# Kernel tuning notes

Measured on AMD Instinct MI355X. Metric: run time of the kernel, lower is better.

The kernel has to match this reference:

```python
import jax, jax.numpy as jnp
import numpy as np

MSE_W, SSIM_W = 0.6, 0.4
WIN, SIGMA = 11, 1.5


def _gaussian_window():
    coords = jnp.arange(WIN, dtype=jnp.float32) - (WIN - 1) / 2.0
    g = jnp.exp(-coords ** 2 / (2.0 * SIGMA ** 2))
    g = g / g.sum()
    w = jnp.outer(g, g)  # [11,11]
    return w.reshape(1, 1, WIN, WIN)  # OIHW


def _blur(x, window):
    # x: [B,1,H,W], valid conv with 11x11 gaussian
    return jax.lax.conv_general_dilated(
        x, window, window_strides=(1, 1), padding='VALID',
        dimension_numbers=('NCHW', 'OIHW', 'NCHW'))


def setup_inputs() -> dict:
    key = jax.random.key(0)
    k1, k2 = jax.random.split(key)
    pred = jax.random.uniform(k1, (32, 1, 512, 512), dtype=jnp.float32)
    target = jax.random.uniform(k2, (32, 1, 512, 512), dtype=jnp.float32)
    return {"pred": pred, "target": target}


def reference(pred, target):
    window = _gaussian_window()
    C1 = (0.01 * 1.0) ** 2
    C2 = (0.03 * 1.0) ** 2

    mse_loss = jnp.mean((pred - target) ** 2)

    mu1 = _blur(pred, window)
    mu2 = _blur(target, window)
    mu1_sq = mu1 * mu1
    mu2_sq = mu2 * mu2
    mu1_mu2 = mu1 * mu2
    sigma1_sq = _blur(pred * pred, window) - mu1_sq
    sigma2_sq = _blur(target * target, window) - mu2_sq
    sigma12 = _blur(pred * target, window) - mu1_mu2

    ssim_map = (2.0 * mu1_mu2 + C1) * (2.0 * sigma12 + C2) / (
        (mu1_sq + mu2_sq + C1) * (sigma1_sq + sigma2_sq + C2) + 1e-6)
    ssim_loss = 1.0 - jnp.mean(ssim_map)

    return MSE_W * mse_loss + SSIM_W * ssim_loss
```

## Files before the change

### kernel.cpp

```cpp
#include <hip/hip_runtime.h>
#include <math.h>

#define BATCH 32
#define H 512
#define W 512
#define OUT_HW 502
#define TS_X 32
#define BAND 32
#define NBANDS 16
#define NTX 16
#define NBLOCKS (NTX * BATCH)
#define N1 ((double)BATCH * H * W)
#define N2 ((double)BATCH * OUT_HW * OUT_HW)

#define RSTR 56
#define TSTR 56

struct GaussW { float g[11]; };

typedef _Float16 h8  __attribute__((ext_vector_type(8)));
typedef __fp16   h2t __attribute__((ext_vector_type(2)));
typedef float    f4t __attribute__((ext_vector_type(4)));

__global__ __launch_bounds__(256, 2)
void ssim_mfma_kernel(const float* __restrict__ pred,
                      const float* __restrict__ targ,
                      float* __restrict__ ws_contrib,
                      GaussW gw)
{
    __shared__ __align__(16) _Float16 raw[4][48 * RSTR];
    __shared__ __align__(16) _Float16 rbt[4][32 * TSTR];
    __shared__ float red[8];

    const int tid = threadIdx.x;
    const int bid = blockIdx.x;
    const int tx  = bid >> 5;
    const int b   = ((bid & 7) << 2) | ((bid >> 3) & 3);
    const int ox0 = tx * TS_X;
    const int cols = min(TS_X, OUT_HW - ox0);
    const bool interior_x = (ox0 + 48 <= W);

    const float* __restrict__ pb = pred + ((size_t)b << 18);
    const float* __restrict__ tb = targ + ((size_t)b << 18);

    const int lane = tid & 63, wave = tid >> 6;
    const int quad = lane >> 4, nn = lane & 15, quad8 = quad << 3;

    const int pr = tid / 6, pg = tid - pr * 6;
    const bool pactive = interior_x | (pg < 4);

    {
        _Float16* base = &raw[0][0];
        const int total = 4 * 48 * RSTR;
        for (int i = tid * 8; i < total; i += 256 * 8)
            *(f4t*)(base + i) = f4t{0.f, 0.f, 0.f, 0.f};
    }

    h8 gfrag;
    #pragma unroll
    for (int j = 0; j < 8; ++j) {
        const int kk = quad8 + j - nn;
        float val = 0.f;
        #pragma unroll
        for (int t2 = 0; t2 < 11; ++t2) val = (kk == t2) ? gw.g[t2] : val;
        gfrag[j] = (_Float16)val;
    }
    const f4t zero4 = {0.f, 0.f, 0.f, 0.f};
    const float C1 = 1e-4f, C2 = 9e-4f;

    float mse_local = 0.f, ssim_local = 0.f;

    f4t pf0, pf1, pf2, pf3;
    {
        const int nnew = 42;
        if ((tid < nnew * 6) & pactive) {
            const int base = (pr << 9) + ox0 + 8 * pg;
            pf0 = *(const f4t*)(pb + base);
            pf1 = *(const f4t*)(pb + base + 4);
            pf2 = *(const f4t*)(tb + base);
            pf3 = *(const f4t*)(tb + base + 4);
        }
    }

    __syncthreads();

    int hbase = 0, obase = 0;

    #pragma unroll 1
    for (int band = 0; band < NBANDS; ++band) {
        const int out0 = band * BAND;
        const int h0   = (band == 0) ? 0 : (out0 + 10);
        const int nnew = min(out0 + 42, H) - h0;

        if ((tid < nnew * 6) & pactive) {
            const h2t hp0 = __builtin_amdgcn_cvt_pkrtz(pf0[0], pf0[1]);
            const h2t hp1 = __builtin_amdgcn_cvt_pkrtz(pf0[2], pf0[3]);
            const h2t hp2 = __builtin_amdgcn_cvt_pkrtz(pf1[0], pf1[1]);
            const h2t hp3 = __builtin_amdgcn_cvt_pkrtz(pf1[2], pf1[3]);
            const h2t ht0 = __builtin_amdgcn_cvt_pkrtz(pf2[0], pf2[1]);
            const h2t ht1 = __builtin_amdgcn_cvt_pkrtz(pf2[2], pf2[3]);
            const h2t ht2 = __builtin_amdgcn_cvt_pkrtz(pf3[0], pf3[1]);
            const h2t ht3 = __builtin_amdgcn_cvt_pkrtz(pf3[2], pf3[3]);
            __align__(16) h2t sv[4], dv[4], ssv[4], ddv[4];
            sv[0] = hp0 + ht0; sv[1] = hp1 + ht1; sv[2] = hp2 + ht2; sv[3] = hp3 + ht3;
            dv[0] = hp0 - ht0; dv[1] = hp1 - ht1; dv[2] = hp2 - ht2; dv[3] = hp3 - ht3;
            ssv[0] = sv[0] * sv[0]; ssv[1] = sv[1] * sv[1];
            ssv[2] = sv[2] * sv[2]; ssv[3] = sv[3] * sv[3];
            ddv[0] = dv[0] * dv[0]; ddv[1] = dv[1] * dv[1];
            ddv[2] = dv[2] * dv[2]; ddv[3] = dv[3] * dv[3];

            if (pg < 4) {
                const h2t macc = (ddv[0] + ddv[1]) + (ddv[2] + ddv[3]);
                mse_local += (float)macc[0] + (float)macc[1];
            }

            int s = hbase + pr;
            s -= (s >= 48) ? 48 : 0;
            const int off = s * RSTR + 8 * pg;
            *(f4t*)&raw[0][off] = *(const f4t*)sv;
            *(f4t*)&raw[1][off] = *(const f4t*)dv;
            *(f4t*)&raw[2][off] = *(const f4t*)ssv;
            *(f4t*)&raw[3][off] = *(const f4t*)ddv;
        }
        __syncthreads();

        if (band + 1 < NBANDS) {
            const int nh0   = out0 + BAND + 10;
            const int nnnew = min(out0 + BAND + 42, H) - nh0;
            if ((tid < nnnew * 6) & pactive) {
                const int base = ((nh0 + pr) << 9) + ox0 + 8 * pg;
                pf0 = *(const f4t*)(pb + base);
                pf1 = *(const f4t*)(pb + base + 4);
                pf2 = *(const f4t*)(tb + base);
                pf3 = *(const f4t*)(tb + base + 4);
            }
        }

        #pragma unroll 1
        for (int t5 = wave; t5 < 24; t5 += 4) {
            const int ch = t5 & 3, rem = t5 >> 2;
            const int j0 = (rem & 1) << 4, r0 = (rem >> 1) << 4;
            int u = obase + r0 + nn;
            u -= (u >= 48) ? 48 : 0;
            const h8 a = *(const h8*)&raw[ch][u * RSTR + j0 + quad8];
            const f4t dacc = __builtin_amdgcn_mfma_f32_16x16x32_f16(a, gfrag, zero4, 0, 0, 0);
            h2t* wp = (h2t*)&rbt[ch][(j0 + nn) * TSTR + r0 + (quad << 2)];
            wp[0] = __builtin_amdgcn_cvt_pkrtz(dacc[0], dacc[1]);
            wp[1] = __builtin_amdgcn_cvt_pkrtz(dacc[2], dacc[3]);
        }
        __syncthreads();

        {
            const int c0 = (wave & 1) << 4, r0v = (wave >> 1) << 4;
            f4t dv2[4];
            #pragma unroll
            for (int ch = 0; ch < 4; ++ch) {
                const h8 a = *(const h8*)&rbt[ch][(c0 + nn) * TSTR + r0v + quad8];
                dv2[ch] = __builtin_amdgcn_mfma_f32_16x16x32_f16(a, gfrag, zero4, 0, 0, 0);
            }
            const int rowg = out0 + r0v + nn;
            if (rowg < OUT_HW) {
                #pragma unroll
                for (int reg = 0; reg < 4; ++reg) {
                    const int cl = c0 + (quad << 2) + reg;
                    if (cl < cols) {
                        const float A = dv2[0][reg], Bv = dv2[1][reg];
                        const float U = dv2[2][reg], V  = dv2[3][reg];
                        const float A2 = A * A, B2 = Bv * Bv;
                        const float mu12_2 = 0.5f * (A2 - B2);
                        const float musq   = 0.5f * (A2 + B2);
                        const float sig12_2 = 0.5f * (U - V) - mu12_2;
                        const float sigsum  = 0.5f * (U + V) - musq;
                        const float num = (mu12_2 + C1) * (sig12_2 + C2);
                        const float den = (musq + C1) * (sigsum + C2) + 1e-6f;
                        ssim_local += num * __builtin_amdgcn_rcpf(den);
                    }
                }
            }
        }

        hbase += nnew;  hbase -= (hbase >= 48) ? 48 : 0;
        obase += BAND;  obase -= (obase >= 48) ? 48 : 0;
    }

    #pragma unroll
    for (int off = 32; off > 0; off >>= 1) {
        ssim_local += __shfl_down(ssim_local, off, 64);
        mse_local  += __shfl_down(mse_local,  off, 64);
    }
    if ((tid & 63) == 0) { red[wave] = ssim_local; red[4 + wave] = mse_local; }
    __syncthreads();
    if (tid == 0) {
        const float s = red[0] + red[1] + red[2] + red[3];
        const float m = red[4] + red[5] + red[6] + red[7];
        const double contrib = 0.6 * (double)m / N1 - 0.4 * (double)s / N2;
        ws_contrib[bid] = (float)contrib;
    }
}

__global__ __launch_bounds__(1024)
void finalize_kernel(const float* __restrict__ ws_contrib,
                     float* __restrict__ out)
{
    __shared__ double rs[1024];
    int tid = threadIdx.x;
    double s = 0.0;
    for (int i = tid; i < NBLOCKS; i += 1024)
        s += (double)ws_contrib[i];
    rs[tid] = s;
    __syncthreads();
    for (int off = 512; off > 0; off >>= 1) {
        if (tid < off) rs[tid] += rs[tid + off];
        __syncthreads();
    }
    if (tid == 0)
        out[0] = (float)(0.4 + rs[0]);
}

extern "C" void kernel_launch(void* const* d_in, const int* in_sizes, int n_in,
                              void* d_out, int out_size, void* d_ws, size_t ws_size,
                              hipStream_t stream)
{
    const float* pred = (const float*)d_in[0];
    const float* targ = (const float*)d_in[1];
    float* out = (float*)d_out;
    float* ws_contrib = (float*)d_ws;

    GaussW gw;
    double g[11], sum = 0.0;
    for (int i = 0; i < 11; ++i) { double x = i - 5.0; g[i] = exp(-x * x / 4.5); sum += g[i]; }
    for (int i = 0; i < 11; ++i) gw.g[i] = (float)(g[i] / sum);

    ssim_mfma_kernel<<<dim3(NBLOCKS), 256, 0, stream>>>(pred, targ, ws_contrib, gw);
    finalize_kernel<<<1, 1024, 0, stream>>>(ws_contrib, out);
}
```

Baseline: 108.4 us.

## Defer vertical blur to next band to drop a barrier, shrink finalize to one wave

The vertical MFMA blur and SSIM accumulation for each band now run at the start of the next band iteration, overlapping the raw-tile staging and global prefetch. This removes one __syncthreads per band. The horizontal pass now assigns one channel per wave with a fully unrolled loop. The finalize kernel becomes a single 64-thread wave doing a shuffle reduction instead of a 1024-thread shared-memory tree. Costs are a trailing epilogue call and more register pressure from inlining the lambda twice.

Result: faster. 102.8 us (-5.1%).

```diff
diff --git a/kernel.cpp b/kernel.cpp
--- a/kernel.cpp
+++ b/kernel.cpp
@@ -70,10 +70,38 @@
 
     float mse_local = 0.f, ssim_local = 0.f;
 
+    auto do_vblur = [&](int out0v) {
+        const int c0 = (wave & 1) << 4, r0v = (wave >> 1) << 4;
+        f4t dv2[4];
+        #pragma unroll
+        for (int ch = 0; ch < 4; ++ch) {
+            const h8 a = *(const h8*)&rbt[ch][(c0 + nn) * TSTR + r0v + quad8];
+            dv2[ch] = __builtin_amdgcn_mfma_f32_16x16x32_f16(a, gfrag, zero4, 0, 0, 0);
+        }
+        const int rowg = out0v + r0v + nn;
+        if (rowg < OUT_HW) {
+            #pragma unroll
+            for (int reg = 0; reg < 4; ++reg) {
+                const int cl = c0 + (quad << 2) + reg;
+                if (cl < cols) {
+                    const float A = dv2[0][reg], Bv = dv2[1][reg];
+                    const float U = dv2[2][reg], V  = dv2[3][reg];
+                    const float A2 = A * A, B2 = Bv * Bv;
+                    const float mu12_2 = 0.5f * (A2 - B2);
+                    const float musq   = 0.5f * (A2 + B2);
+                    const float sig12_2 = 0.5f * (U - V) - mu12_2;
+                    const float sigsum  = 0.5f * (U + V) - musq;
+                    const float num = (mu12_2 + C1) * (sig12_2 + C2);
+                    const float den = (musq + C1) * (sigsum + C2) + 1e-6f;
+                    ssim_local += num * __builtin_amdgcn_rcpf(den);
+                }
+            }
+        }
+    };
+
     f4t pf0, pf1, pf2, pf3;
     {
-        const int nnew = 42;
-        if ((tid < nnew * 6) & pactive) {
+        if ((tid < 42 * 6) & pactive) {
             const int base = (pr << 9) + ox0 + 8 * pg;
             pf0 = *(const f4t*)(pb + base);
             pf1 = *(const f4t*)(pb + base + 4);
@@ -91,6 +119,8 @@
         const int out0 = band * BAND;
         const int h0   = (band == 0) ? 0 : (out0 + 10);
         const int nnew = min(out0 + 42, H) - h0;
+
+        if (band > 0) do_vblur(out0 - BAND);
 
         if ((tid < nnew * 6) & pactive) {
             const h2t hp0 = __builtin_amdgcn_cvt_pkrtz(pf0[0], pf0[1]);
@@ -122,7 +152,6 @@
             *(f4t*)&raw[2][off] = *(const f4t*)ssv;
             *(f4t*)&raw[3][off] = *(const f4t*)ddv;
         }
-        __syncthreads();
 
         if (band + 1 < NBANDS) {
             const int nh0   = out0 + BAND + 10;
@@ -135,53 +164,26 @@
                 pf3 = *(const f4t*)(tb + base + 4);
             }
         }
-
-        #pragma unroll 1
-        for (int t5 = wave; t5 < 24; t5 += 4) {
-            const int ch = t5 & 3, rem = t5 >> 2;
-            const int j0 = (rem & 1) << 4, r0 = (rem >> 1) << 4;
+        __syncthreads();
+
+        #pragma unroll
+        for (int k = 0; k < 6; ++k) {
+            const int j0 = (k & 1) << 4, r0 = (k >> 1) << 4;
             int u = obase + r0 + nn;
             u -= (u >= 48) ? 48 : 0;
-            const h8 a = *(const h8*)&raw[ch][u * RSTR + j0 + quad8];
+            const h8 a = *(const h8*)&raw[wave][u * RSTR + j0 + quad8];
             const f4t dacc = __builtin_amdgcn_mfma_f32_16x16x32_f16(a, gfrag, zero4, 0, 0, 0);
-            h2t* wp = (h2t*)&rbt[ch][(j0 + nn) * TSTR + r0 + (quad << 2)];
+            h2t* wp = (h2t*)&rbt[wave][(j0 + nn) * TSTR + r0 + (quad << 2)];
             wp[0] = __builtin_amdgcn_cvt_pkrtz(dacc[0], dacc[1]);
             wp[1] = __builtin_amdgcn_cvt_pkrtz(dacc[2], dacc[3]);
         }
         __syncthreads();
 
-        {
-            const int c0 = (wave & 1) << 4, r0v = (wave >> 1) << 4;
-            f4t dv2[4];
-            #pragma unroll
-            for (int ch = 0; ch < 4; ++ch) {
-                const h8 a = *(const h8*)&rbt[ch][(c0 + nn) * TSTR + r0v + quad8];
-                dv2[ch] = __builtin_amdgcn_mfma_f32_16x16x32_f16(a, gfrag, zero4, 0, 0, 0);
-            }
-            const int rowg = out0 + r0v + nn;
-            if (rowg < OUT_HW) {
-                #pragma unroll
-                for (int reg = 0; reg < 4; ++reg) {
-                    const int cl = c0 + (quad << 2) + reg;
-                    if (cl < cols) {
-                        const float A = dv2[0][reg], Bv = dv2[1][reg];
-                        const float U = dv2[2][reg], V  = dv2[3][reg];
-                        const float A2 = A * A, B2 = Bv * Bv;
-                        const float mu12_2 = 0.5f * (A2 - B2);
-                        const float musq   = 0.5f * (A2 + B2);
-                        const float sig12_2 = 0.5f * (U - V) - mu12_2;
-                        const float sigsum  = 0.5f * (U + V) - musq;
-                        const float num = (mu12_2 + C1) * (sig12_2 + C2);
-                        const float den = (musq + C1) * (sigsum + C2) + 1e-6f;
-                        ssim_local += num * __builtin_amdgcn_rcpf(den);
-                    }
-                }
-            }
-        }
-
         hbase += nnew;  hbase -= (hbase >= 48) ? 48 : 0;
         obase += BAND;  obase -= (obase >= 48) ? 48 : 0;
     }
+
+    do_vblur((NBANDS - 1) * BAND);
 
     #pragma unroll
     for (int off = 32; off > 0; off >>= 1) {
@@ -198,23 +200,20 @@
     }
 }
 
-__global__ __launch_bounds__(1024)
+__global__ __launch_bounds__(64)
 void finalize_kernel(const float* __restrict__ ws_contrib,
                      float* __restrict__ out)
 {
-    __shared__ double rs[1024];
-    int tid = threadIdx.x;
+    const int tid = threadIdx.x;
     double s = 0.0;
-    for (int i = tid; i < NBLOCKS; i += 1024)
-        s += (double)ws_contrib[i];
-    rs[tid] = s;
-    __syncthreads();
-    for (int off = 512; off > 0; off >>= 1) {
-        if (tid < off) rs[tid] += rs[tid + off];
-        __syncthreads();
-    }
+    #pragma unroll
+    for (int i = 0; i < NBLOCKS / 64; ++i)
+        s += (double)ws_contrib[tid + i * 64];
+    #pragma unroll
+    for (int off = 32; off > 0; off >>= 1)
+        s += __shfl_down(s, off, 64);
     if (tid == 0)
-        out[0] = (float)(0.4 + rs[0]);
+        out[0] = (float)(0.4 + s);
 }
 
 extern "C" void kernel_launch(void* const* d_in, const int* in_sizes, int n_in,
@@ -232,5 +231,5 @@
     for (int i = 0; i < 11; ++i) gw.g[i] = (float)(g[i] / sum);
 
     ssim_mfma_kernel<<<dim3(NBLOCKS), 256, 0, stream>>>(pred, targ, ws_contrib, gw);
-    finalize_kernel<<<1, 1024, 0, stream>>>(ws_contrib, out);
+    finalize_kernel<<<1, 64, 0, stream>>>(ws_contrib, out);
 }
```
